# Optimization experiments

Measured on AMD Instinct MI355X. Metric: run time of the kernel, lower is better.

## Reference

```python
import jax, jax.numpy as jnp
import numpy as np

CODEBOOK_SIZE = 8192
EMBED_DIM = 128
BETA = 0.25


def setup_inputs() -> dict:
    key = jax.random.key(0)
    k1, k2, k3, k4 = jax.random.split(key, 4)
    z = jax.random.normal(k1, (8, 4096, EMBED_DIM), dtype=jnp.float32)
    # nn.Embedding init: normal(0, D**-0.5), frozen
    emb_weight = jax.random.normal(k2, (CODEBOOK_SIZE, EMBED_DIM), dtype=jnp.float32) * (EMBED_DIM ** -0.5)
    # nn.Linear default init scale ~ 1/sqrt(in_features)
    lim = 1.0 / np.sqrt(EMBED_DIM)
    proj_w = jax.random.uniform(k3, (EMBED_DIM, EMBED_DIM), jnp.float32, -lim, lim)
    proj_b = jax.random.uniform(k4, (EMBED_DIM,), jnp.float32, -lim, lim)
    return {"z": z, "emb_weight": emb_weight, "proj_w": proj_w, "proj_b": proj_b}


def reference(z, emb_weight, proj_w, proj_b):
    z_flat = z.reshape(-1, EMBED_DIM)  # [T, D]
    # embedding_proj: Linear -> codebook @ W^T + b
    quant_codebook = emb_weight @ proj_w.T + proj_b  # [K, D]
    # squared distances: |z|^2 + |c|^2 - 2 z c^T  -> [T, K]
    d = (jnp.sum(z_flat ** 2, axis=1, keepdims=True)
         + jnp.sum(quant_codebook ** 2, axis=1)
         - 2.0 * jnp.einsum('td,kd->tk', z_flat, quant_codebook))
    idx = jnp.argmin(d, axis=1)  # [T]
    z_q = quant_codebook[idx].reshape(z.shape)
    # codebook usage / perplexity
    counts = jax.ops.segment_sum(jnp.ones_like(idx, dtype=jnp.float32), idx,
                                 num_segments=CODEBOOK_SIZE)
    e_mean = counts / idx.shape[0]
    perplexity = jnp.exp(-jnp.sum(e_mean * jnp.log(e_mean + 1e-8)))
    sg = jax.lax.stop_gradient
    commit_loss = (BETA * jnp.mean((sg(z_q) - z) ** 2)
                   + jnp.mean((z_q - sg(z)) ** 2))
    z_q_st = z + sg(z_q - z)  # straight-through estimator
    return (z_q_st, commit_loss, perplexity)
```

## Files before the change

### kernel.cpp

```cpp
#include <hip/hip_runtime.h>
#include <math.h>

#define T_TOK 32768
#define D_DIM 128
#define K_CODE 8192
#define BM 256
#define BN 64

typedef unsigned long long ull;
typedef _Float16 v8h __attribute__((ext_vector_type(8)));
typedef _Float16 v4h __attribute__((ext_vector_type(4)));
typedef float v16f __attribute__((ext_vector_type(16)));

#define SCALE 4096.0f
#define DESCALE (1.0f / 4096.0f)
#define ACC_SCALE (-0x1p-23f)


__global__ __launch_bounds__(256) void proj_kernel(const float* __restrict__ E,
                                                  const float* __restrict__ W,
                                                  const float* __restrict__ b,
                                                  char* __restrict__ Cpack,
                                                  float* __restrict__ cn) {
    int r = blockIdx.x * 4 + (threadIdx.x >> 6);
    int l = threadIdx.x & 63;
    const float4* E4 = (const float4*)(E + (size_t)r * D_DIM);
    const float4* WA = (const float4*)(W + (size_t)l * D_DIM);
    const float4* WB = (const float4*)(W + (size_t)(l + 64) * D_DIM);

    float4 aA = make_float4(0.f, 0.f, 0.f, 0.f);
    float4 aB = make_float4(0.f, 0.f, 0.f, 0.f);
#pragma unroll
    for (int dd = 0; dd < 32; ++dd) {
        float4 e = E4[dd];
        float4 wa = WA[dd], wb = WB[dd];
        aA.x = fmaf(e.x, wa.x, aA.x);
        aA.y = fmaf(e.y, wa.y, aA.y);
        aA.z = fmaf(e.z, wa.z, aA.z);
        aA.w = fmaf(e.w, wa.w, aA.w);
        aB.x = fmaf(e.x, wb.x, aB.x);
        aB.y = fmaf(e.y, wb.y, aB.y);
        aB.z = fmaf(e.z, wb.z, aB.z);
        aB.w = fmaf(e.w, wb.w, aB.w);
    }
    float vA = ((aA.x + aA.y) + (aA.z + aA.w)) + b[l];
    float vB = ((aB.x + aB.y) + (aB.z + aB.w)) + b[l + 64];

    char* cp = Cpack + (size_t)(r >> 6) * 32768;
    int mt = (r >> 5) & 1, rs = r & 31;
    {
        int kc = l >> 4, hf = (l >> 3) & 1, j = l & 7;
        float f = vA * SCALE;
        _Float16 h = (_Float16)f;
        _Float16 m = (_Float16)(f - (float)h);
        size_t off = (size_t)((mt * 8 + kc) * 1024 + (hf * 32 + rs) * 16 + j * 2);
        *(_Float16*)(cp + off) = h;
        *(_Float16*)(cp + off + 16384) = m;
    }
    {
        int d = l + 64;
        int kc = d >> 4, hf = (d >> 3) & 1, j = d & 7;
        float f = vB * SCALE;
        _Float16 h = (_Float16)f;
        _Float16 m = (_Float16)(f - (float)h);
        size_t off = (size_t)((mt * 8 + kc) * 1024 + (hf * 32 + rs) * 16 + j * 2);
        *(_Float16*)(cp + off) = h;
        *(_Float16*)(cp + off + 16384) = m;
    }

    float s = vA * vA + vB * vB;
#pragma unroll
    for (int off = 32; off > 0; off >>= 1) s += __shfl_down(s, off, 64);
    if (l == 0) cn[r] = s;
}

__global__ __launch_bounds__(256) void prep_z_kernel(const float* __restrict__ Z,
                                                     char* __restrict__ Zpack,
                                                     ull* __restrict__ packed,
                                                     int* __restrict__ counts) {
    int tb = blockIdx.x;
    int tid = threadIdx.x;
    int lane = tid & 63;
    int w = tid >> 6;

    int g = blockIdx.x * 256 + tid;
    if (g < T_TOK) packed[g] = ~0ull;
    if (g < K_CODE) counts[g] = 0;

    char* zp = Zpack + (size_t)tb * 16384;
#pragma unroll
    for (int kq = 0; kq < 2; ++kq) {
        int kc = 2 * w + kq;
        const float* src = Z + (size_t)(tb * 32 + (lane & 31)) * D_DIM
                             + kc * 16 + (lane >> 5) * 8;
        float4 a = *(const float4*)(src);
        float4 c = *(const float4*)(src + 4);
        float vals[8] = {a.x, a.y, a.z, a.w, c.x, c.y, c.z, c.w};
        v8h h, m;
#pragma unroll
        for (int j = 0; j < 8; ++j) {
            float f = vals[j] * SCALE;
            _Float16 hh = (_Float16)f;
            h[j] = hh;
            m[j] = (_Float16)(f - (float)hh);
        }
        *(v8h*)(zp + (size_t)(kc * 1024 + lane * 16)) = h;
        *(v8h*)(zp + (size_t)(8192 + kc * 1024 + lane * 16)) = m;
    }
}

__global__ __launch_bounds__(256, 3) void argmin_kernel(const char* __restrict__ Zpack,
                                                        const char* __restrict__ Cpack,
                                                        const float* __restrict__ cn,
                                                        ull* __restrict__ packed) {
    __shared__ __align__(16) char lds[33024];

    int tid = threadIdx.x;
    int lane = tid & 63;
    int w = tid >> 6;
    int half_id = lane >> 5;

    int bid = blockIdx.x;
    int xcd = bid & 7;
    int q = bid >> 3;
    int cb = q & 127;
    int win = xcd + 8 * (q >> 7);
    int nb = cb * BN;
    int mb = win * BM;

    {
        const char* src = Cpack + (size_t)cb * 32768;
#pragma unroll
        for (int it = 0; it < 8; ++it) {
            int off = it * 4096 + tid * 16;
            __builtin_amdgcn_global_load_lds(
                (const __attribute__((address_space(1))) void*)(src + off),
                (__attribute__((address_space(3))) void*)(lds + off),
                16, 0, 0);
        }
        if (tid < 64) ((float*)(lds + 32768))[tid] = cn[nb + tid];
    }

    int tbw = (mb >> 5) + 2 * w;
    const char* zb0 = Zpack + (size_t)tbw * 16384 + lane * 16;

    v8h pb[4][3];
#pragma unroll
    for (int n = 0; n < 2; ++n) {
        pb[2 * n + 0][0] = *(const v8h*)(zb0 + n * 16384);
        pb[2 * n + 1][0] = *(const v8h*)(zb0 + n * 16384 + 8192);
        pb[2 * n + 0][1] = *(const v8h*)(zb0 + n * 16384 + 1024);
        pb[2 * n + 1][1] = *(const v8h*)(zb0 + n * 16384 + 8192 + 1024);
    }

    __syncthreads();

    const char* ab = lds + lane * 16;
    const float* cn_s = (const float*)(lds + 32768);

    v16f acc[2][2];
#pragma unroll
    for (int mt = 0; mt < 2; ++mt)
#pragma unroll
        for (int n = 0; n < 2; ++n) acc[mt][n] = (v16f)0.f;

#pragma unroll
    for (int kc = 0; kc < 8; ++kc) {
        int curb = kc % 3;

        if (kc < 6) {
            int slot = (kc + 2) % 3;
#pragma unroll
            for (int n = 0; n < 2; ++n) {
                pb[2 * n + 0][slot] = *(const v8h*)(zb0 + n * 16384 + (kc + 2) * 1024);
                pb[2 * n + 1][slot] = *(const v8h*)(zb0 + n * 16384 + 8192 + (kc + 2) * 1024);
            }
        }

        v8h Ah0 = *(const v8h*)(ab + (0 * 8 + kc) * 1024);
        v8h Ah1 = *(const v8h*)(ab + (1 * 8 + kc) * 1024);

        __builtin_amdgcn_s_setprio(1);
#pragma unroll
        for (int n = 0; n < 2; ++n)
            acc[0][n] = __builtin_amdgcn_mfma_f32_32x32x16_f16(Ah0, pb[2 * n][curb], acc[0][n], 0, 0, 0);
#pragma unroll
        for (int n = 0; n < 2; ++n)
            acc[1][n] = __builtin_amdgcn_mfma_f32_32x32x16_f16(Ah1, pb[2 * n][curb], acc[1][n], 0, 0, 0);
#pragma unroll
        for (int n = 0; n < 2; ++n)
            acc[0][n] = __builtin_amdgcn_mfma_f32_32x32x16_f16(Ah0, pb[2 * n + 1][curb], acc[0][n], 0, 0, 0);
#pragma unroll
        for (int n = 0; n < 2; ++n)
            acc[1][n] = __builtin_amdgcn_mfma_f32_32x32x16_f16(Ah1, pb[2 * n + 1][curb], acc[1][n], 0, 0, 0);
        __builtin_amdgcn_s_setprio(0);

        v8h Am0 = *(const v8h*)(ab + (2 * 8 + kc) * 1024);
        v8h Am1 = *(const v8h*)(ab + (3 * 8 + kc) * 1024);

        __builtin_amdgcn_s_setprio(1);
#pragma unroll
        for (int n = 0; n < 2; ++n)
            acc[0][n] = __builtin_amdgcn_mfma_f32_32x32x16_f16(Am0, pb[2 * n][curb], acc[0][n], 0, 0, 0);
#pragma unroll
        for (int n = 0; n < 2; ++n)
            acc[1][n] = __builtin_amdgcn_mfma_f32_32x32x16_f16(Am1, pb[2 * n][curb], acc[1][n], 0, 0, 0);
        __builtin_amdgcn_s_setprio(0);
    }

    float best[2];
    int bi[2];
#pragma unroll
    for (int n = 0; n < 2; ++n) { best[n] = 3.4e38f; bi[n] = nb; }

#pragma unroll
    for (int mt = 0; mt < 2; ++mt) {
        float cnreg[16];
#pragma unroll
        for (int reg = 0; reg < 16; ++reg) {
            int mrow = 32 * mt + (reg & 3) + 8 * (reg >> 2) + 4 * half_id;
            cnreg[reg] = cn_s[mrow];
        }
#pragma unroll
        for (int n = 0; n < 2; ++n) {
#pragma unroll
            for (int reg = 0; reg < 16; ++reg) {
                int mrow = 32 * mt + (reg & 3) + 8 * (reg >> 2) + 4 * half_id;
                int code = nb + mrow;
                float s = fmaf(acc[mt][n][reg], ACC_SCALE, cnreg[reg]);
                if (s < best[n]) { best[n] = s; bi[n] = code; }
            }
        }
    }

#pragma unroll
    for (int n = 0; n < 2; ++n) {
        float ob = __shfl_xor(best[n], 32, 64);
        int oi = __shfl_xor(bi[n], 32, 64);
        if (ob < best[n] || (ob == best[n] && oi < bi[n])) { best[n] = ob; bi[n] = oi; }
        if ((n & 1) == half_id) {
            int tok = mb + w * 64 + n * 32 + (lane & 31);
            unsigned ub = __float_as_uint(best[n]);
            unsigned key = ub ^ ((unsigned)(((int)ub) >> 31) | 0x80000000u);
            ull pk = ((ull)key << 32) | (unsigned)bi[n];
            atomicMin(&packed[tok], pk);
        }
    }
}

__global__ __launch_bounds__(256) void zq_kernel(const float* __restrict__ Z,
                                                 const char* __restrict__ Cpack,
                                                 const ull* __restrict__ packed,
                                                 float* __restrict__ out,
                                                 int* __restrict__ counts,
                                                 float* __restrict__ lpart) {
    int gid = blockIdx.x * 256 + threadIdx.x;
    int t = gid >> 5;
    int d4 = gid & 31;
    int idx = (int)(packed[t] & 0xFFFFFFFFull);
    if (d4 == 0) atomicAdd(&counts[idx], 1);

    int d0 = 4 * d4;
    int kc = d0 >> 4, hf = (d0 >> 3) & 1, j0 = d0 & 7;
    const char* cp = Cpack + (size_t)(idx >> 6) * 32768
                   + (size_t)((((idx >> 5) & 1) * 8 + kc) * 1024
                              + (hf * 32 + (idx & 31)) * 16 + j0 * 2);
    v4h h = *(const v4h*)(cp);
    v4h m = *(const v4h*)(cp + 16384);
    float4 cv;
    cv.x = ((float)h[0] + (float)m[0]) * DESCALE;
    cv.y = ((float)h[1] + (float)m[1]) * DESCALE;
    cv.z = ((float)h[2] + (float)m[2]) * DESCALE;
    cv.w = ((float)h[3] + (float)m[3]) * DESCALE;

    float4 zv = ((const float4*)Z)[gid];
    float dx = cv.x - zv.x, dy = cv.y - zv.y, dz = cv.z - zv.z, dw = cv.w - zv.w;
    float4 o;
    o.x = zv.x + dx;
    o.y = zv.y + dy;
    o.z = zv.z + dz;
    o.w = zv.w + dw;
    ((float4*)out)[gid] = o;

    float ls = dx * dx + dy * dy + dz * dz + dw * dw;
#pragma unroll
    for (int off = 32; off > 0; off >>= 1) ls += __shfl_down(ls, off, 64);
    __shared__ float red[4];
    int lane = threadIdx.x & 63, w = threadIdx.x >> 6;
    if (lane == 0) red[w] = ls;
    __syncthreads();
    if (threadIdx.x == 0) lpart[blockIdx.x] = (red[0] + red[1]) + (red[2] + red[3]);
}

__global__ __launch_bounds__(256) void scalars_kernel(const int* __restrict__ counts,
                                                      const float* __restrict__ lpart,
                                                      float* __restrict__ out) {
    float s = 0.f;
    for (int i = threadIdx.x; i < K_CODE; i += 256) {
        float e = (float)counts[i] * (1.0f / (float)T_TOK);
        s += e * logf(e + 1e-8f);
    }
    float ls = 0.f;
    for (int i = threadIdx.x; i < 4096; i += 256) ls += lpart[i];
#pragma unroll
    for (int off = 32; off > 0; off >>= 1) {
        s += __shfl_down(s, off, 64);
        ls += __shfl_down(ls, off, 64);
    }
    __shared__ float red[8];
    int lane = threadIdx.x & 63, w = threadIdx.x >> 6;
    if (lane == 0) { red[w] = s; red[4 + w] = ls; }
    __syncthreads();
    if (threadIdx.x == 0) {
        float ssum = (red[0] + red[1]) + (red[2] + red[3]);
        float lsum = (red[4] + red[5]) + (red[6] + red[7]);
        out[(size_t)T_TOK * D_DIM + 0] = 1.25f * lsum / (float)((size_t)T_TOK * D_DIM);
        out[(size_t)T_TOK * D_DIM + 1] = expf(-ssum);
    }
}

extern "C" void kernel_launch(void* const* d_in, const int* in_sizes, int n_in,
                              void* d_out, int out_size, void* d_ws, size_t ws_size,
                              hipStream_t stream) {
    const float* z   = (const float*)d_in[0];
    const float* emb = (const float*)d_in[1];
    const float* pw  = (const float*)d_in[2];
    const float* pb  = (const float*)d_in[3];
    float* out = (float*)d_out;

    char* Zpack = (char*)d_out;

    char* ws = (char*)d_ws;
    char*  Cpack  = ws + 0;
    float* cn     = (float*)(ws + 4194304);
    float* lpart  = (float*)(ws + 4227072);
    ull*   packed = (ull*)  (ws + 4358144);
    int*   counts = (int*)  (ws + 4620288);

    proj_kernel<<<K_CODE / 4, 256, 0, stream>>>(emb, pw, pb, Cpack, cn);
    prep_z_kernel<<<T_TOK / 32, 256, 0, stream>>>(z, Zpack, packed, counts);
    argmin_kernel<<<(K_CODE / BN) * (T_TOK / BM), 256, 0, stream>>>(Zpack, Cpack, cn, packed);
    zq_kernel<<<(T_TOK * D_DIM / 4) / 256, 256, 0, stream>>>(z, Cpack, packed, out, counts, lpart);
    scalars_kernel<<<1, 256, 0, stream>>>(counts, lpart, out);
}
```

Measured before the change: 369.3 us.

## Merge projection and z-prep kernels; double-buffer LDS A-fragment loads in argmin

Merges the codebook projection kernel and the z packing kernel into one launch, with block index ranges selecting the role. This removes one kernel launch and lets the two independent prep jobs run concurrently. In the argmin MFMA loop, all four A fragments for the next k-chunk are now prefetched from LDS into a double-buffered register array, so LDS reads overlap the current MFMAs. The cost is more VGPR pressure, which may hurt occupancy under the launch bound of 3 blocks per unit.

Result: no change. 370.3 us, median of 2 (+0.3%).

```diff
diff --git a/kernel.cpp b/kernel.cpp
--- a/kernel.cpp
+++ b/kernel.cpp
@@ -17,95 +17,96 @@
 #define ACC_SCALE (-0x1p-23f)
 
 
-__global__ __launch_bounds__(256) void proj_kernel(const float* __restrict__ E,
-                                                  const float* __restrict__ W,
-                                                  const float* __restrict__ b,
-                                                  char* __restrict__ Cpack,
-                                                  float* __restrict__ cn) {
-    int r = blockIdx.x * 4 + (threadIdx.x >> 6);
-    int l = threadIdx.x & 63;
-    const float4* E4 = (const float4*)(E + (size_t)r * D_DIM);
-    const float4* WA = (const float4*)(W + (size_t)l * D_DIM);
-    const float4* WB = (const float4*)(W + (size_t)(l + 64) * D_DIM);
-
-    float4 aA = make_float4(0.f, 0.f, 0.f, 0.f);
-    float4 aB = make_float4(0.f, 0.f, 0.f, 0.f);
-#pragma unroll
-    for (int dd = 0; dd < 32; ++dd) {
-        float4 e = E4[dd];
-        float4 wa = WA[dd], wb = WB[dd];
-        aA.x = fmaf(e.x, wa.x, aA.x);
-        aA.y = fmaf(e.y, wa.y, aA.y);
-        aA.z = fmaf(e.z, wa.z, aA.z);
-        aA.w = fmaf(e.w, wa.w, aA.w);
-        aB.x = fmaf(e.x, wb.x, aB.x);
-        aB.y = fmaf(e.y, wb.y, aB.y);
-        aB.z = fmaf(e.z, wb.z, aB.z);
-        aB.w = fmaf(e.w, wb.w, aB.w);
-    }
-    float vA = ((aA.x + aA.y) + (aA.z + aA.w)) + b[l];
-    float vB = ((aB.x + aB.y) + (aB.z + aB.w)) + b[l + 64];
-
-    char* cp = Cpack + (size_t)(r >> 6) * 32768;
-    int mt = (r >> 5) & 1, rs = r & 31;
-    {
-        int kc = l >> 4, hf = (l >> 3) & 1, j = l & 7;
-        float f = vA * SCALE;
-        _Float16 h = (_Float16)f;
-        _Float16 m = (_Float16)(f - (float)h);
-        size_t off = (size_t)((mt * 8 + kc) * 1024 + (hf * 32 + rs) * 16 + j * 2);
-        *(_Float16*)(cp + off) = h;
-        *(_Float16*)(cp + off + 16384) = m;
-    }
-    {
-        int d = l + 64;
-        int kc = d >> 4, hf = (d >> 3) & 1, j = d & 7;
-        float f = vB * SCALE;
-        _Float16 h = (_Float16)f;
-        _Float16 m = (_Float16)(f - (float)h);
-        size_t off = (size_t)((mt * 8 + kc) * 1024 + (hf * 32 + rs) * 16 + j * 2);
-        *(_Float16*)(cp + off) = h;
-        *(_Float16*)(cp + off + 16384) = m;
-    }
-
-    float s = vA * vA + vB * vB;
-#pragma unroll
-    for (int off = 32; off > 0; off >>= 1) s += __shfl_down(s, off, 64);
-    if (l == 0) cn[r] = s;
-}
-
-__global__ __launch_bounds__(256) void prep_z_kernel(const float* __restrict__ Z,
-                                                     char* __restrict__ Zpack,
-                                                     ull* __restrict__ packed,
-                                                     int* __restrict__ counts) {
-    int tb = blockIdx.x;
+__global__ __launch_bounds__(256) void prep_kernel(const float* __restrict__ E,
+                                                   const float* __restrict__ W,
+                                                   const float* __restrict__ b,
+                                                   char* __restrict__ Cpack,
+                                                   float* __restrict__ cn,
+                                                   const float* __restrict__ Z,
+                                                   char* __restrict__ Zpack,
+                                                   ull* __restrict__ packed,
+                                                   int* __restrict__ counts) {
     int tid = threadIdx.x;
     int lane = tid & 63;
-    int w = tid >> 6;
-
-    int g = blockIdx.x * 256 + tid;
-    if (g < T_TOK) packed[g] = ~0ull;
-    if (g < K_CODE) counts[g] = 0;
-
-    char* zp = Zpack + (size_t)tb * 16384;
-#pragma unroll
-    for (int kq = 0; kq < 2; ++kq) {
-        int kc = 2 * w + kq;
-        const float* src = Z + (size_t)(tb * 32 + (lane & 31)) * D_DIM
-                             + kc * 16 + (lane >> 5) * 8;
-        float4 a = *(const float4*)(src);
-        float4 c = *(const float4*)(src + 4);
-        float vals[8] = {a.x, a.y, a.z, a.w, c.x, c.y, c.z, c.w};
-        v8h h, m;
-#pragma unroll
-        for (int j = 0; j < 8; ++j) {
-            float f = vals[j] * SCALE;
-            _Float16 hh = (_Float16)f;
-            h[j] = hh;
-            m[j] = (_Float16)(f - (float)hh);
-        }
-        *(v8h*)(zp + (size_t)(kc * 1024 + lane * 16)) = h;
-        *(v8h*)(zp + (size_t)(8192 + kc * 1024 + lane * 16)) = m;
+    if (blockIdx.x < 2048) {
+        int r = blockIdx.x * 4 + (tid >> 6);
+        int l = lane;
+        const float4* E4 = (const float4*)(E + (size_t)r * D_DIM);
+        const float4* WA = (const float4*)(W + (size_t)l * D_DIM);
+        const float4* WB = (const float4*)(W + (size_t)(l + 64) * D_DIM);
+
+        float4 aA = make_float4(0.f, 0.f, 0.f, 0.f);
+        float4 aB = make_float4(0.f, 0.f, 0.f, 0.f);
+#pragma unroll
+        for (int dd = 0; dd < 32; ++dd) {
+            float4 e = E4[dd];
+            float4 wa = WA[dd], wb = WB[dd];
+            aA.x = fmaf(e.x, wa.x, aA.x);
+            aA.y = fmaf(e.y, wa.y, aA.y);
+            aA.z = fmaf(e.z, wa.z, aA.z);
+            aA.w = fmaf(e.w, wa.w, aA.w);
+            aB.x = fmaf(e.x, wb.x, aB.x);
+            aB.y = fmaf(e.y, wb.y, aB.y);
+            aB.z = fmaf(e.z, wb.z, aB.z);
+            aB.w = fmaf(e.w, wb.w, aB.w);
+        }
+        float vA = ((aA.x + aA.y) + (aA.z + aA.w)) + b[l];
+        float vB = ((aB.x + aB.y) + (aB.z + aB.w)) + b[l + 64];
+
+        char* cp = Cpack + (size_t)(r >> 6) * 32768;
+        int mt = (r >> 5) & 1, rs = r & 31;
+        {
+            int kc = l >> 4, hf = (l >> 3) & 1, j = l & 7;
+            float f = vA * SCALE;
+            _Float16 h = (_Float16)f;
+            _Float16 m = (_Float16)(f - (float)h);
+            size_t off = (size_t)((mt * 8 + kc) * 1024 + (hf * 32 + rs) * 16 + j * 2);
+            *(_Float16*)(cp + off) = h;
+            *(_Float16*)(cp + off + 16384) = m;
+        }
+        {
+            int d = l + 64;
+            int kc = d >> 4, hf = (d >> 3) & 1, j = d & 7;
+            float f = vB * SCALE;
+            _Float16 h = (_Float16)f;
+            _Float16 m = (_Float16)(f - (float)h);
+            size_t off = (size_t)((mt * 8 + kc) * 1024 + (hf * 32 + rs) * 16 + j * 2);
+            *(_Float16*)(cp + off) = h;
+            *(_Float16*)(cp + off + 16384) = m;
+        }
+
+        float s = vA * vA + vB * vB;
+#pragma unroll
+        for (int off = 32; off > 0; off >>= 1) s += __shfl_down(s, off, 64);
+        if (l == 0) cn[r] = s;
+    } else {
+        int tb = blockIdx.x - 2048;
+        int w = tid >> 6;
+
+        int g = tb * 256 + tid;
+        if (g < T_TOK) packed[g] = ~0ull;
+        if (g < K_CODE) counts[g] = 0;
+
+        char* zp = Zpack + (size_t)tb * 16384;
+#pragma unroll
+        for (int kq = 0; kq < 2; ++kq) {
+            int kc = 2 * w + kq;
+            const float* src = Z + (size_t)(tb * 32 + (lane & 31)) * D_DIM
+                                 + kc * 16 + (lane >> 5) * 8;
+            float4 a = *(const float4*)(src);
+            float4 c = *(const float4*)(src + 4);
+            float vals[8] = {a.x, a.y, a.z, a.w, c.x, c.y, c.z, c.w};
+            v8h h, m;
+#pragma unroll
+            for (int j = 0; j < 8; ++j) {
+                float f = vals[j] * SCALE;
+                _Float16 hh = (_Float16)f;
+                h[j] = hh;
+                m[j] = (_Float16)(f - (float)hh);
+            }
+            *(v8h*)(zp + (size_t)(kc * 1024 + lane * 16)) = h;
+            *(v8h*)(zp + (size_t)(8192 + kc * 1024 + lane * 16)) = m;
+        }
     }
 }
 
@@ -164,9 +165,21 @@
 #pragma unroll
         for (int n = 0; n < 2; ++n) acc[mt][n] = (v16f)0.f;
 
+    v8h Af[2][4];
+#pragma unroll
+    for (int f = 0; f < 4; ++f)
+        Af[0][f] = *(const v8h*)(ab + (f * 8 + 0) * 1024);
+
 #pragma unroll
     for (int kc = 0; kc < 8; ++kc) {
         int curb = kc % 3;
+        int cura = kc & 1;
+
+        if (kc < 7) {
+#pragma unroll
+            for (int f = 0; f < 4; ++f)
+                Af[cura ^ 1][f] = *(const v8h*)(ab + (f * 8 + kc + 1) * 1024);
+        }
 
         if (kc < 6) {
             int slot = (kc + 2) % 3;
@@ -177,34 +190,25 @@
             }
         }
 
-        v8h Ah0 = *(const v8h*)(ab + (0 * 8 + kc) * 1024);
-        v8h Ah1 = *(const v8h*)(ab + (1 * 8 + kc) * 1024);
-
         __builtin_amdgcn_s_setprio(1);
 #pragma unroll
         for (int n = 0; n < 2; ++n)
-            acc[0][n] = __builtin_amdgcn_mfma_f32_32x32x16_f16(Ah0, pb[2 * n][curb], acc[0][n], 0, 0, 0);
-#pragma unroll
-        for (int n = 0; n < 2; ++n)
-            acc[1][n] = __builtin_amdgcn_mfma_f32_32x32x16_f16(Ah1, pb[2 * n][curb], acc[1][n], 0, 0, 0);
-#pragma unroll
-        for (int n = 0; n < 2; ++n)
-            acc[0][n] = __builtin_amdgcn_mfma_f32_32x32x16_f16(Ah0, pb[2 * n + 1][curb], acc[0][n], 0, 0, 0);
-#pragma unroll
-        for (int n = 0; n < 2; ++n)
-            acc[1][n] = __builtin_amdgcn_mfma_f32_32x32x16_f16(Ah1, pb[2 * n + 1][curb], acc[1][n], 0, 0, 0);
-        __builtin_amdgcn_s_setprio(0);
-
-        v8h Am0 = *(const v8h*)(ab + (2 * 8 + kc) * 1024);
-        v8h Am1 = *(const v8h*)(ab + (3 * 8 + kc) * 1024);
-
-        __builtin_amdgcn_s_setprio(1);
-#pragma unroll
-        for (int n = 0; n < 2; ++n)
-            acc[0][n] = __builtin_amdgcn_mfma_f32_32x32x16_f16(Am0, pb[2 * n][curb], acc[0][n], 0, 0, 0);
-#pragma unroll
-        for (int n = 0; n < 2; ++n)
-            acc[1][n] = __builtin_amdgcn_mfma_f32_32x32x16_f16(Am1, pb[2 * n][curb], acc[1][n], 0, 0, 0);
+            acc[0][n] = __builtin_amdgcn_mfma_f32_32x32x16_f16(Af[cura][0], pb[2 * n][curb], acc[0][n], 0, 0, 0);
+#pragma unroll
+        for (int n = 0; n < 2; ++n)
+            acc[1][n] = __builtin_amdgcn_mfma_f32_32x32x16_f16(Af[cura][1], pb[2 * n][curb], acc[1][n], 0, 0, 0);
+#pragma unroll
+        for (int n = 0; n < 2; ++n)
+            acc[0][n] = __builtin_amdgcn_mfma_f32_32x32x16_f16(Af[cura][0], pb[2 * n + 1][curb], acc[0][n], 0, 0, 0);
+#pragma unroll
+        for (int n = 0; n < 2; ++n)
+            acc[1][n] = __builtin_amdgcn_mfma_f32_32x32x16_f16(Af[cura][1], pb[2 * n + 1][curb], acc[1][n], 0, 0, 0);
+#pragma unroll
+        for (int n = 0; n < 2; ++n)
+            acc[0][n] = __builtin_amdgcn_mfma_f32_32x32x16_f16(Af[cura][2], pb[2 * n][curb], acc[0][n], 0, 0, 0);
+#pragma unroll
+        for (int n = 0; n < 2; ++n)
+            acc[1][n] = __builtin_amdgcn_mfma_f32_32x32x16_f16(Af[cura][3], pb[2 * n][curb], acc[1][n], 0, 0, 0);
         __builtin_amdgcn_s_setprio(0);
     }
 
@@ -337,8 +341,7 @@
     ull*   packed = (ull*)  (ws + 4358144);
     int*   counts = (int*)  (ws + 4620288);
 
-    proj_kernel<<<K_CODE / 4, 256, 0, stream>>>(emb, pw, pb, Cpack, cn);
-    prep_z_kernel<<<T_TOK / 32, 256, 0, stream>>>(z, Zpack, packed, counts);
+    prep_kernel<<<3072, 256, 0, stream>>>(emb, pw, pb, Cpack, cn, z, Zpack, packed, counts);
     argmin_kernel<<<(K_CODE / BN) * (T_TOK / BM), 256, 0, stream>>>(Zpack, Cpack, cn, packed);
     zq_kernel<<<(T_TOK * D_DIM / 4) / 256, 256, 0, stream>>>(z, Cpack, packed, out, counts, lpart);
     scalars_kernel<<<1, 256, 0, stream>>>(counts, lpart, out);
```
